# Kernel optimization log

Hardware: AMD Instinct MI355X
Metric: run time of the kernel (lower is better)

## Reference

```python
import jax, jax.numpy as jnp
import numpy as np

N, E, R, D_IN, D_OUT = 50000, 800000, 8, 64, 64


def setup_inputs() -> dict:
    key = jax.random.key(0)
    ks = jax.random.split(key, 8)
    feat = jax.random.normal(ks[0], (N, D_IN), dtype=jnp.float32)
    edge_src = jax.random.randint(ks[1], (E,), 0, N, dtype=jnp.int32)
    edge_dst = jax.random.randint(ks[2], (E,), 0, N, dtype=jnp.int32)
    etype = jax.random.randint(ks[3], (E,), 0, R, dtype=jnp.int32)
    attention = jax.random.uniform(ks[4], (E, 1), dtype=jnp.float32)
    weight = jax.random.normal(ks[5], (R, D_IN, D_OUT), dtype=jnp.float32) * (6.0 / (D_IN + D_OUT)) ** 0.5
    h_bias = jnp.zeros((D_OUT,), dtype=jnp.float32)
    loop_weight = jax.random.normal(ks[6], (D_IN, D_OUT), dtype=jnp.float32) * (6.0 / (D_IN + D_OUT)) ** 0.5
    return {"feat": feat, "edge_src": edge_src, "edge_dst": edge_dst,
            "etype": etype, "attention": attention, "weight": weight,
            "h_bias": h_bias, "loop_weight": loop_weight}


def reference(feat, edge_src, edge_dst, etype, attention, weight, h_bias, loop_weight):
    # Project all nodes through every relation weight once: [R, N, D_OUT].
    # (Equivalent to per-edge bmm with weight[etype] on gathered src feats,
    #  but avoids materializing a [E, D_IN, D_OUT] weight tensor.)
    proj = jnp.einsum('ni,rio->rno', feat, weight)
    # Per-edge message: gather relation-specific projection of src node.
    m = (proj[etype, edge_src] + h_bias) * attention          # [E, D_OUT]
    # Scatter-sum messages to destination nodes.
    agg = jax.ops.segment_sum(m, edge_dst, num_segments=feat.shape[0])
    # Self-loop.
    return agg + feat @ loop_weight
```

## Files before the change

kernel.cpp:

```cpp
#include <hip/hip_runtime.h>

#define D 64

typedef unsigned short ushort_t;
typedef __attribute__((ext_vector_type(8))) short bf16x8;
typedef __attribute__((ext_vector_type(4))) float f32x4;

__device__ __forceinline__ void fma4(float4& c, float a, const float4& b) {
  c.x = fmaf(a, b.x, c.x);
  c.y = fmaf(a, b.y, c.y);
  c.z = fmaf(a, b.z, c.z);
  c.w = fmaf(a, b.w, c.w);
}

__device__ __forceinline__ unsigned short f2bf(float f) {
  unsigned u = __float_as_uint(f);
  return (unsigned short)((u + 0x7FFFu + ((u >> 16) & 1u)) >> 16);
}
__device__ __forceinline__ float bf2f(unsigned short h) {
  return __uint_as_float((unsigned)h << 16);
}
__device__ __forceinline__ unsigned pk2(float a, float b) {
  return (unsigned)f2bf(a) | ((unsigned)f2bf(b) << 16);
}

__device__ __forceinline__ bf16x8 pack_bf8(float4 v0, float4 v1) {
  bf16x8 r;
  r[0] = (short)f2bf(v0.x); r[1] = (short)f2bf(v0.y);
  r[2] = (short)f2bf(v0.z); r[3] = (short)f2bf(v0.w);
  r[4] = (short)f2bf(v1.x); r[5] = (short)f2bf(v1.y);
  r[6] = (short)f2bf(v1.z); r[7] = (short)f2bf(v1.w);
  return r;
}

__global__ void prep(const float* __restrict__ weight, const float* __restrict__ loopw,
                     ushort_t* __restrict__ Wt, int* __restrict__ deg, int R, int N) {
  if ((int)blockIdx.x <= R) {
    const int m = blockIdx.x;
    const float* W = (m < R) ? weight + (size_t)m * D * D : loopw;
    ushort_t* o = Wt + (size_t)m * D * D;
    for (int i = threadIdx.x; i < 1024; i += 256) {
      float4 v = ((const float4*)W)[i];
      int k = i >> 4;
      int c = (i & 15) * 4;
      o[(c + 0) * D + k] = f2bf(v.x);
      o[(c + 1) * D + k] = f2bf(v.y);
      o[(c + 2) * D + k] = f2bf(v.z);
      o[(c + 3) * D + k] = f2bf(v.w);
    }
  } else {
    int i = (blockIdx.x - (R + 1)) * 256 + threadIdx.x;
    if (i < N) deg[i] = 0;
  }
}

template <int NM>
__device__ __forceinline__ void proj_body(const float* __restrict__ feat,
                                          const ushort_t* __restrict__ Wt,
                                          ushort_t* __restrict__ proj,
                                          float* __restrict__ out, int N, int blk) {
  const int t = threadIdx.x;
  const int lane = t & 63;
  const int wid = t >> 6;
  const int node = blk * 64 + wid * 16 + (lane & 15);
  const int g = lane >> 4;
  const int kb = g * 8;
  const int R8 = NM - 1;

  bf16x8 b0, b1;
  {
    float4 v0 = make_float4(0.f, 0.f, 0.f, 0.f), v1 = v0, v2 = v0, v3 = v0;
    if (node < N) {
      const float* p = feat + (size_t)node * D + kb;
      v0 = *(const float4*)p;
      v1 = *(const float4*)(p + 4);
      v2 = *(const float4*)(p + 32);
      v3 = *(const float4*)(p + 36);
    }
    b0 = pack_bf8(v0, v1);
    b1 = pack_bf8(v2, v3);
  }

#pragma unroll 2
  for (int m = 0; m < NM; ++m) {
    const ushort_t* wt = Wt + (size_t)m * D * D + kb;
    f32x4 acc[4];
#pragma unroll
    for (int ct = 0; ct < 4; ++ct) {
      const ushort_t* wr = wt + (size_t)(16 * ct + (lane & 15)) * D;
      bf16x8 a0 = *(const bf16x8*)wr;
      bf16x8 a1 = *(const bf16x8*)(wr + 32);
      acc[ct] = (f32x4){0.f, 0.f, 0.f, 0.f};
      acc[ct] = __builtin_amdgcn_mfma_f32_16x16x32_bf16(a0, b0, acc[ct], 0, 0, 0);
      acc[ct] = __builtin_amdgcn_mfma_f32_16x16x32_bf16(a1, b1, acc[ct], 0, 0, 0);
    }
    if (node < N) {
      if (m < R8) {
        ushort_t* op = proj + ((size_t)node * R8 + m) * D + 16 * g;
        uint4 w0, w1;
        w0.x = pk2(acc[0][0], acc[0][1]); w0.y = pk2(acc[0][2], acc[0][3]);
        w0.z = pk2(acc[1][0], acc[1][1]); w0.w = pk2(acc[1][2], acc[1][3]);
        w1.x = pk2(acc[2][0], acc[2][1]); w1.y = pk2(acc[2][2], acc[2][3]);
        w1.z = pk2(acc[3][0], acc[3][1]); w1.w = pk2(acc[3][2], acc[3][3]);
        *(uint4*)(op) = w0;
        *(uint4*)(op + 8) = w1;
      } else {
        float* op = out + (size_t)node * D + 4 * g;
#pragma unroll
        for (int ct = 0; ct < 4; ++ct) {
          float4 v;
          v.x = acc[ct][0]; v.y = acc[ct][1]; v.z = acc[ct][2]; v.w = acc[ct][3];
          *(float4*)(op + 16 * ct) = v;
        }
      }
    }
  }
}

__device__ __forceinline__ void proj_body_rt(const float* __restrict__ feat,
                                             const ushort_t* __restrict__ Wt,
                                             ushort_t* __restrict__ proj,
                                             float* __restrict__ out, int N, int R,
                                             int blk) {
  const int t = threadIdx.x;
  const int lane = t & 63;
  const int wid = t >> 6;
  const int node = blk * 64 + wid * 16 + (lane & 15);
  const int g = lane >> 4;
  const int kb = g * 8;

  bf16x8 b0, b1;
  {
    float4 v0 = make_float4(0.f, 0.f, 0.f, 0.f), v1 = v0, v2 = v0, v3 = v0;
    if (node < N) {
      const float* p = feat + (size_t)node * D + kb;
      v0 = *(const float4*)p;
      v1 = *(const float4*)(p + 4);
      v2 = *(const float4*)(p + 32);
      v3 = *(const float4*)(p + 36);
    }
    b0 = pack_bf8(v0, v1);
    b1 = pack_bf8(v2, v3);
  }

  for (int m = 0; m <= R; ++m) {
    const ushort_t* wt = Wt + (size_t)m * D * D + kb;
    f32x4 acc[4];
#pragma unroll
    for (int ct = 0; ct < 4; ++ct) {
      const ushort_t* wr = wt + (size_t)(16 * ct + (lane & 15)) * D;
      bf16x8 a0 = *(const bf16x8*)wr;
      bf16x8 a1 = *(const bf16x8*)(wr + 32);
      acc[ct] = (f32x4){0.f, 0.f, 0.f, 0.f};
      acc[ct] = __builtin_amdgcn_mfma_f32_16x16x32_bf16(a0, b0, acc[ct], 0, 0, 0);
      acc[ct] = __builtin_amdgcn_mfma_f32_16x16x32_bf16(a1, b1, acc[ct], 0, 0, 0);
    }
    if (node < N) {
      if (m < R) {
        ushort_t* op = proj + ((size_t)node * R + m) * D + 16 * g;
        uint4 w0, w1;
        w0.x = pk2(acc[0][0], acc[0][1]); w0.y = pk2(acc[0][2], acc[0][3]);
        w0.z = pk2(acc[1][0], acc[1][1]); w0.w = pk2(acc[1][2], acc[1][3]);
        w1.x = pk2(acc[2][0], acc[2][1]); w1.y = pk2(acc[2][2], acc[2][3]);
        w1.z = pk2(acc[3][0], acc[3][1]); w1.w = pk2(acc[3][2], acc[3][3]);
        *(uint4*)(op) = w0;
        *(uint4*)(op + 8) = w1;
      } else {
        float* op = out + (size_t)node * D + 4 * g;
#pragma unroll
        for (int ct = 0; ct < 4; ++ct) {
          float4 v;
          v.x = acc[ct][0]; v.y = acc[ct][1]; v.z = acc[ct][2]; v.w = acc[ct][3];
          *(float4*)(op + 16 * ct) = v;
        }
      }
    }
  }
}

__device__ __forceinline__ void hist_body(const int* __restrict__ edst,
                                          int* __restrict__ deg,
                                          int* __restrict__ rank, int E, int hblk) {
  const int e = (hblk * 256 + (int)threadIdx.x) * 4;
  if (e + 3 < E) {
    int4 d = *(const int4*)(edst + e);
    int4 r;
    r.x = atomicAdd(&deg[d.x], 1);
    r.y = atomicAdd(&deg[d.y], 1);
    r.z = atomicAdd(&deg[d.z], 1);
    r.w = atomicAdd(&deg[d.w], 1);
    *(int4*)(rank + e) = r;
  } else {
    for (int i = e; i < E; ++i) rank[i] = atomicAdd(&deg[edst[i]], 1);
  }
}

__global__ __launch_bounds__(256) void proj_hist(const float* __restrict__ feat,
                                                 const ushort_t* __restrict__ Wt,
                                                 ushort_t* __restrict__ proj,
                                                 float* __restrict__ out,
                                                 const int* __restrict__ edst,
                                                 int* __restrict__ deg,
                                                 int* __restrict__ rank,
                                                 int N, int E, int R, int PB) {
  if ((int)blockIdx.x < PB) {
    if (R == 8)
      proj_body<9>(feat, Wt, proj, out, N, blockIdx.x);
    else
      proj_body_rt(feat, Wt, proj, out, N, R, blockIdx.x);
  } else {
    hist_body(edst, deg, rank, E, blockIdx.x - PB);
  }
}

__global__ __launch_bounds__(256) void scan_partial(const int* __restrict__ deg,
                                                    int* __restrict__ bsum, int N) {
  const int t = threadIdx.x;
  const int base = blockIdx.x * 1024 + t * 4;
  int s = 0;
  if (base + 3 < N) {
    int4 v = *(const int4*)(deg + base);
    s = v.x + v.y + v.z + v.w;
  } else {
#pragma unroll
    for (int k = 0; k < 4; ++k) if (base + k < N) s += deg[base + k];
  }
  __shared__ int red[4];
#pragma unroll
  for (int m = 1; m < 64; m <<= 1) s += __shfl_xor(s, m);
  if ((t & 63) == 0) red[t >> 6] = s;
  __syncthreads();
  if (t == 0) bsum[blockIdx.x] = red[0] + red[1] + red[2] + red[3];
}

__global__ __launch_bounds__(256) void scan_bsum(const int* __restrict__ bsum,
                                                 int* __restrict__ boff,
                                                 int* __restrict__ off, int nb, int N) {
  __shared__ int s[256];
  __shared__ int carry_s;
  const int t = threadIdx.x;
  if (t == 0) carry_s = 0;
  __syncthreads();
  for (int base = 0; base < nb; base += 256) {
    int i = base + t;
    int v = (i < nb) ? bsum[i] : 0;
    s[t] = v;
    __syncthreads();
#pragma unroll
    for (int d = 1; d < 256; d <<= 1) {
      int u = (t >= d) ? s[t - d] : 0;
      __syncthreads();
      s[t] += u;
      __syncthreads();
    }
    int c = carry_s;
    if (i < nb) boff[i] = s[t] - v + c;
    __syncthreads();
    if (t == 0) carry_s = c + s[255];
    __syncthreads();
  }
  if (t == 0) off[N] = carry_s;
}

__global__ __launch_bounds__(256) void scan_apply(const int* __restrict__ deg,
                                                  const int* __restrict__ boff,
                                                  int* __restrict__ off, int N) {
  const int t = threadIdx.x;
  const int base = blockIdx.x * 1024 + t * 4;
  int v0 = 0, v1 = 0, v2 = 0, v3 = 0;
  if (base + 3 < N) {
    int4 v = *(const int4*)(deg + base);
    v0 = v.x; v1 = v.y; v2 = v.z; v3 = v.w;
  } else {
    if (base + 0 < N) v0 = deg[base + 0];
    if (base + 1 < N) v1 = deg[base + 1];
    if (base + 2 < N) v2 = deg[base + 2];
  }
  const int tsum = v0 + v1 + v2 + v3;
  __shared__ int s[256];
  s[t] = tsum;
  __syncthreads();
#pragma unroll
  for (int d = 1; d < 256; d <<= 1) {
    int u = (t >= d) ? s[t - d] : 0;
    __syncthreads();
    s[t] += u;
    __syncthreads();
  }
  int exc = s[t] - tsum + boff[blockIdx.x];
  const int o1 = exc + v0, o2 = o1 + v1, o3 = o2 + v2;
  if (base + 0 < N) off[base + 0] = exc;
  if (base + 1 < N) off[base + 1] = o1;
  if (base + 2 < N) off[base + 2] = o2;
  if (base + 3 < N) off[base + 3] = o3;
}

__global__ void scatter_pos(const int* __restrict__ esrc, const int* __restrict__ edst,
                            const int* __restrict__ etype, const float* __restrict__ att,
                            const int* __restrict__ off, const int* __restrict__ rank,
                            int2* __restrict__ payload, int E) {
  const int e = (blockIdx.x * 256 + threadIdx.x) * 4;
  if (e + 3 < E) {
    int4 s  = *(const int4*)(esrc + e);
    int4 d  = *(const int4*)(edst + e);
    int4 ty = *(const int4*)(etype + e);
    float4 a = *(const float4*)(att + e);
    int4 rk = *(const int4*)(rank + e);
    payload[off[d.x] + rk.x] = make_int2(s.x | (ty.x << 24), __float_as_int(a.x));
    payload[off[d.y] + rk.y] = make_int2(s.y | (ty.y << 24), __float_as_int(a.y));
    payload[off[d.z] + rk.z] = make_int2(s.z | (ty.z << 24), __float_as_int(a.z));
    payload[off[d.w] + rk.w] = make_int2(s.w | (ty.w << 24), __float_as_int(a.w));
  } else {
    for (int i = e; i < E; ++i)
      payload[off[edst[i]] + rank[i]] =
          make_int2(esrc[i] | (etype[i] << 24), __float_as_int(att[i]));
  }
}

__global__ __launch_bounds__(256, 8) void node_gather(const int* __restrict__ off,
                                                      const int2* __restrict__ payload,
                                                      const ushort_t* __restrict__ proj,
                                                      const float* __restrict__ hbias,
                                                      float* __restrict__ out, int N,
                                                      int R) {
  const int n = (blockIdx.x * 256 + threadIdx.x) >> 6;
  if (n >= N) return;
  const int lane = threadIdx.x & 63;
  const int sub = lane >> 4;
  const int q = lane & 15;
  const int ac0 = 16 * (q & 3) + 4 * (q >> 2);

  const int s0 = off[n], s1 = off[n + 1];
  float4 acc = make_float4(0.f, 0.f, 0.f, 0.f);
  float sa = 0.f;
  for (int e = s0 + sub; e < s1; e += 4) {
    const int2 pe = payload[e];
    const float a = __int_as_float(pe.y);
    const int src = pe.x & 0x00FFFFFF;
    const int r = ((unsigned)pe.x) >> 24;
    const ushort4 p = *(const ushort4*)(proj + ((size_t)src * R + r) * D + q * 4);
    acc.x = fmaf(a, bf2f(p.x), acc.x);
    acc.y = fmaf(a, bf2f(p.y), acc.y);
    acc.z = fmaf(a, bf2f(p.z), acc.z);
    acc.w = fmaf(a, bf2f(p.w), acc.w);
    sa += a;
  }
#pragma unroll
  for (int m = 16; m < 64; m <<= 1) {
    acc.x += __shfl_xor(acc.x, m);
    acc.y += __shfl_xor(acc.y, m);
    acc.z += __shfl_xor(acc.z, m);
    acc.w += __shfl_xor(acc.w, m);
    sa += __shfl_xor(sa, m);
  }
  if (sub == 0) {
    const float4 hb = *(const float4*)(hbias + ac0);
    float* op = out + (size_t)n * D + ac0;
    float4 cur = *(float4*)op;
    cur.x += acc.x + sa * hb.x;
    cur.y += acc.y + sa * hb.y;
    cur.z += acc.z + sa * hb.z;
    cur.w += acc.w + sa * hb.w;
    *(float4*)op = cur;
  }
}

__global__ __launch_bounds__(256, 3) void proj_single(const float* __restrict__ feat,
                                                      const float* __restrict__ W,
                                                      float* __restrict__ outp, int N) {
  __shared__ float sW[64 * 64];
  __shared__ float sF[64 * 132];
  const int t = threadIdx.x;
  const int tileBase = blockIdx.x * 128;

  {
    const float4* Wv = (const float4*)W;
    float4* sWv = (float4*)sW;
    for (int k = t; k < 1024; k += 256) sWv[k] = Wv[k];
  }
  {
    const int row = t >> 1, half = t & 1;
    const int gr = tileBase + row;
    if (gr < N) {
      const float4* src = (const float4*)(feat + (size_t)gr * D + half * 32);
#pragma unroll
      for (int k = 0; k < 8; ++k) {
        float4 v = src[k];
        int i0 = half * 32 + k * 4;
        sF[(i0 + 0) * 132 + row] = v.x;
        sF[(i0 + 1) * 132 + row] = v.y;
        sF[(i0 + 2) * 132 + row] = v.z;
        sF[(i0 + 3) * 132 + row] = v.w;
      }
    } else {
#pragma unroll
      for (int k = 0; k < 8; ++k) {
        int i0 = half * 32 + k * 4;
        sF[(i0 + 0) * 132 + row] = 0.f;
        sF[(i0 + 1) * 132 + row] = 0.f;
        sF[(i0 + 2) * 132 + row] = 0.f;
        sF[(i0 + 3) * 132 + row] = 0.f;
      }
    }
  }
  __syncthreads();

  const int c0 = (t & 15) * 4;
  const int r0 = (t >> 4) * 8;
  float4 acc[8];
#pragma unroll
  for (int rr = 0; rr < 8; ++rr) acc[rr] = make_float4(0.f, 0.f, 0.f, 0.f);

#pragma unroll 8
  for (int i = 0; i < 64; ++i) {
    float4 w  = *(const float4*)&sW[i * 64 + c0];
    float4 a0 = *(const float4*)&sF[i * 132 + r0];
    float4 a1 = *(const float4*)&sF[i * 132 + r0 + 4];
    fma4(acc[0], a0.x, w); fma4(acc[1], a0.y, w);
    fma4(acc[2], a0.z, w); fma4(acc[3], a0.w, w);
    fma4(acc[4], a1.x, w); fma4(acc[5], a1.y, w);
    fma4(acc[6], a1.z, w); fma4(acc[7], a1.w, w);
  }

#pragma unroll
  for (int rr = 0; rr < 8; ++rr) {
    int gn = tileBase + r0 + rr;
    if (gn < N) *(float4*)(outp + (size_t)gn * D + c0) = acc[rr];
  }
}

__global__ __launch_bounds__(256, 8) void edge_scatter(const int* __restrict__ esrc,
                                                       const int* __restrict__ edst,
                                                       const int* __restrict__ etype,
                                                       const float* __restrict__ att,
                                                       const float* __restrict__ proj,
                                                       const float* __restrict__ hbias,
                                                       float* __restrict__ out,
                                                       int E, int N, int relFilter) {
  const int t = blockIdx.x * 256 + threadIdx.x;
  const int wave = t >> 6;
  const int lane = threadIdx.x & 63;
  const int sub = lane >> 4;
  const int q = lane & 15;
  const long e = (long)wave * 4 + sub;
  if (e >= E) return;
  const int r = etype[e];
  if (relFilter >= 0 && r != relFilter) return;
  const int s = esrc[e];
  const int dn = edst[e];
  const float a = att[e];
  const size_t base = (size_t)s * D;
  const float4 hb = ((const float4*)hbias)[q];
  const float4 p = *(const float4*)(proj + base + q * 4);
  float* op = out + (size_t)dn * D + q * 4;
  unsafeAtomicAdd(op + 0, (p.x + hb.x) * a);
  unsafeAtomicAdd(op + 1, (p.y + hb.y) * a);
  unsafeAtomicAdd(op + 2, (p.z + hb.z) * a);
  unsafeAtomicAdd(op + 3, (p.w + hb.w) * a);
}

extern "C" void kernel_launch(void* const* d_in, const int* in_sizes, int n_in,
                              void* d_out, int out_size, void* d_ws, size_t ws_size,
                              hipStream_t stream) {
  const float* feat   = (const float*)d_in[0];
  const int* esrc     = (const int*)d_in[1];
  const int* edst     = (const int*)d_in[2];
  const int* etype    = (const int*)d_in[3];
  const float* att    = (const float*)d_in[4];
  const float* weight = (const float*)d_in[5];
  const float* hbias  = (const float*)d_in[6];
  const float* loopw  = (const float*)d_in[7];
  float* out = (float*)d_out;

  const int N = in_sizes[0] / D;
  const int E = in_sizes[1];
  const int R = in_sizes[5] / (D * D);

  const int Npad = (N + 3) & ~3;
  const int nb = (N + 1023) / 1024;

  const size_t wtBytes   = (size_t)(R + 1) * D * D * 2;
  const size_t projBytes = (size_t)N * R * D * 2;
  const size_t intCount  = (size_t)Npad + (size_t)(N + 1) + (size_t)nb + (size_t)E;
  const size_t payOff    = (wtBytes + projBytes + intCount * 4 + 7) & ~(size_t)7;
  const size_t needSorted = payOff + (size_t)E * 8;

  const int PB = (N + 63) / 64;
  const int HB = ((E + 3) / 4 + 255) / 256;
  const int equadBlocks = ((E + 3) / 4 + 255) / 256;

  if (ws_size >= needSorted) {
    ushort_t* Wt   = (ushort_t*)d_ws;
    ushort_t* proj = (ushort_t*)((char*)d_ws + wtBytes);
    int* deg    = (int*)((char*)d_ws + wtBytes + projBytes);
    int* off    = deg + Npad;
    int* bsum   = off + (N + 1);
    int* rank   = bsum + nb;
    int2* payload = (int2*)((char*)d_ws + payOff);

    prep<<<(R + 1) + (N + 255) / 256, 256, 0, stream>>>(weight, loopw, Wt, deg, R, N);
    proj_hist<<<PB + HB, 256, 0, stream>>>(feat, Wt, proj, out, edst, deg, rank,
                                           N, E, R, PB);
    scan_partial<<<nb, 256, 0, stream>>>(deg, bsum, N);
    scan_bsum<<<1, 256, 0, stream>>>(bsum, bsum, off, nb, N);
    scan_apply<<<nb, 256, 0, stream>>>(deg, bsum, off, N);
    scatter_pos<<<equadBlocks, 256, 0, stream>>>(esrc, edst, etype, att, off, rank,
                                                 payload, E);
    node_gather<<<(N + 3) / 4, 256, 0, stream>>>(off, payload, proj, hbias, out, N, R);
  } else {
    const int tilesN = (N + 127) / 128;
    const int eblocks16 = (E + 15) / 16;
    proj_single<<<tilesN, 256, 0, stream>>>(feat, loopw, out, N);
    for (int r = 0; r < R; ++r) {
      proj_single<<<tilesN, 256, 0, stream>>>(feat, weight + (size_t)r * D * D,
                                              (float*)d_ws, N);
      edge_scatter<<<eblocks16, 256, 0, stream>>>(esrc, edst, etype, att, (float*)d_ws,
                                                  hbias, out, E, N, r);
    }
  }
}
```

Baseline: 121.6 us.

## Replace CSR sort with fixed-capacity per-node slot buckets and overflow list

Drops the degree histogram, the three-kernel prefix scan and the separate positional scatter. Edges are now binned directly into fixed 48-slot buckets per destination node using an atomic cursor, inside the same launch as the projection. Edges beyond the capacity go to an overflow list that a small atomic-add kernel applies after the gather. This cuts several launches and passes over the edge arrays, at the cost of a larger, sparser payload buffer. Overflow entries past the list cap would be silently dropped, so very skewed degree distributions are a correctness risk.

```diff
diff --git a/kernel.cpp b/kernel.cpp
--- a/kernel.cpp
+++ b/kernel.cpp
@@ -1,6 +1,8 @@
 #include <hip/hip_runtime.h>
 
 #define D 64
+#define CAP 48
+#define OVCAP 8192
 
 typedef unsigned short ushort_t;
 typedef __attribute__((ext_vector_type(8))) short bf16x8;
@@ -34,7 +36,8 @@
 }
 
 __global__ void prep(const float* __restrict__ weight, const float* __restrict__ loopw,
-                     ushort_t* __restrict__ Wt, int* __restrict__ deg, int R, int N) {
+                     ushort_t* __restrict__ Wt, int* __restrict__ cursor,
+                     int* __restrict__ ovcnt, int R, int N) {
   if ((int)blockIdx.x <= R) {
     const int m = blockIdx.x;
     const float* W = (m < R) ? weight + (size_t)m * D * D : loopw;
@@ -48,9 +51,10 @@
       o[(c + 2) * D + k] = f2bf(v.z);
       o[(c + 3) * D + k] = f2bf(v.w);
     }
+    if (blockIdx.x == 0 && threadIdx.x == 0) *ovcnt = 0;
   } else {
     int i = (blockIdx.x - (R + 1)) * 256 + threadIdx.x;
-    if (i < N) deg[i] = 0;
+    if (i < N) cursor[i] = 0;
   }
 }
 
@@ -178,146 +182,69 @@
   }
 }
 
-__device__ __forceinline__ void hist_body(const int* __restrict__ edst,
-                                          int* __restrict__ deg,
-                                          int* __restrict__ rank, int E, int hblk) {
-  const int e = (hblk * 256 + (int)threadIdx.x) * 4;
-  if (e + 3 < E) {
-    int4 d = *(const int4*)(edst + e);
-    int4 r;
-    r.x = atomicAdd(&deg[d.x], 1);
-    r.y = atomicAdd(&deg[d.y], 1);
-    r.z = atomicAdd(&deg[d.z], 1);
-    r.w = atomicAdd(&deg[d.w], 1);
-    *(int4*)(rank + e) = r;
-  } else {
-    for (int i = e; i < E; ++i) rank[i] = atomicAdd(&deg[edst[i]], 1);
-  }
-}
-
-__global__ __launch_bounds__(256) void proj_hist(const float* __restrict__ feat,
-                                                 const ushort_t* __restrict__ Wt,
-                                                 ushort_t* __restrict__ proj,
-                                                 float* __restrict__ out,
-                                                 const int* __restrict__ edst,
-                                                 int* __restrict__ deg,
-                                                 int* __restrict__ rank,
-                                                 int N, int E, int R, int PB) {
-  if ((int)blockIdx.x < PB) {
-    if (R == 8)
-      proj_body<9>(feat, Wt, proj, out, N, blockIdx.x);
-    else
-      proj_body_rt(feat, Wt, proj, out, N, R, blockIdx.x);
-  } else {
-    hist_body(edst, deg, rank, E, blockIdx.x - PB);
-  }
-}
-
-__global__ __launch_bounds__(256) void scan_partial(const int* __restrict__ deg,
-                                                    int* __restrict__ bsum, int N) {
-  const int t = threadIdx.x;
-  const int base = blockIdx.x * 1024 + t * 4;
-  int s = 0;
-  if (base + 3 < N) {
-    int4 v = *(const int4*)(deg + base);
-    s = v.x + v.y + v.z + v.w;
-  } else {
-#pragma unroll
-    for (int k = 0; k < 4; ++k) if (base + k < N) s += deg[base + k];
-  }
-  __shared__ int red[4];
-#pragma unroll
-  for (int m = 1; m < 64; m <<= 1) s += __shfl_xor(s, m);
-  if ((t & 63) == 0) red[t >> 6] = s;
-  __syncthreads();
-  if (t == 0) bsum[blockIdx.x] = red[0] + red[1] + red[2] + red[3];
-}
-
-__global__ __launch_bounds__(256) void scan_bsum(const int* __restrict__ bsum,
-                                                 int* __restrict__ boff,
-                                                 int* __restrict__ off, int nb, int N) {
-  __shared__ int s[256];
-  __shared__ int carry_s;
-  const int t = threadIdx.x;
-  if (t == 0) carry_s = 0;
-  __syncthreads();
-  for (int base = 0; base < nb; base += 256) {
-    int i = base + t;
-    int v = (i < nb) ? bsum[i] : 0;
-    s[t] = v;
-    __syncthreads();
-#pragma unroll
-    for (int d = 1; d < 256; d <<= 1) {
-      int u = (t >= d) ? s[t - d] : 0;
-      __syncthreads();
-      s[t] += u;
-      __syncthreads();
-    }
-    int c = carry_s;
-    if (i < nb) boff[i] = s[t] - v + c;
-    __syncthreads();
-    if (t == 0) carry_s = c + s[255];
-    __syncthreads();
-  }
-  if (t == 0) off[N] = carry_s;
-}
-
-__global__ __launch_bounds__(256) void scan_apply(const int* __restrict__ deg,
-                                                  const int* __restrict__ boff,
-                                                  int* __restrict__ off, int N) {
-  const int t = threadIdx.x;
-  const int base = blockIdx.x * 1024 + t * 4;
-  int v0 = 0, v1 = 0, v2 = 0, v3 = 0;
-  if (base + 3 < N) {
-    int4 v = *(const int4*)(deg + base);
-    v0 = v.x; v1 = v.y; v2 = v.z; v3 = v.w;
-  } else {
-    if (base + 0 < N) v0 = deg[base + 0];
-    if (base + 1 < N) v1 = deg[base + 1];
-    if (base + 2 < N) v2 = deg[base + 2];
-  }
-  const int tsum = v0 + v1 + v2 + v3;
-  __shared__ int s[256];
-  s[t] = tsum;
-  __syncthreads();
-#pragma unroll
-  for (int d = 1; d < 256; d <<= 1) {
-    int u = (t >= d) ? s[t - d] : 0;
-    __syncthreads();
-    s[t] += u;
-    __syncthreads();
-  }
-  int exc = s[t] - tsum + boff[blockIdx.x];
-  const int o1 = exc + v0, o2 = o1 + v1, o3 = o2 + v2;
-  if (base + 0 < N) off[base + 0] = exc;
-  if (base + 1 < N) off[base + 1] = o1;
-  if (base + 2 < N) off[base + 2] = o2;
-  if (base + 3 < N) off[base + 3] = o3;
-}
-
-__global__ void scatter_pos(const int* __restrict__ esrc, const int* __restrict__ edst,
-                            const int* __restrict__ etype, const float* __restrict__ att,
-                            const int* __restrict__ off, const int* __restrict__ rank,
-                            int2* __restrict__ payload, int E) {
-  const int e = (blockIdx.x * 256 + threadIdx.x) * 4;
+__device__ __forceinline__ void scat_body(const int* __restrict__ esrc,
+                                          const int* __restrict__ edst,
+                                          const int* __restrict__ etype,
+                                          const float* __restrict__ att,
+                                          int* __restrict__ cursor,
+                                          int2* __restrict__ payload,
+                                          int* __restrict__ ovcnt,
+                                          int4* __restrict__ ovlist,
+                                          int E, int sblk) {
+  const int e = (sblk * 256 + (int)threadIdx.x) * 4;
   if (e + 3 < E) {
     int4 s  = *(const int4*)(esrc + e);
     int4 d  = *(const int4*)(edst + e);
     int4 ty = *(const int4*)(etype + e);
     float4 a = *(const float4*)(att + e);
-    int4 rk = *(const int4*)(rank + e);
-    payload[off[d.x] + rk.x] = make_int2(s.x | (ty.x << 24), __float_as_int(a.x));
-    payload[off[d.y] + rk.y] = make_int2(s.y | (ty.y << 24), __float_as_int(a.y));
-    payload[off[d.z] + rk.z] = make_int2(s.z | (ty.z << 24), __float_as_int(a.z));
-    payload[off[d.w] + rk.w] = make_int2(s.w | (ty.w << 24), __float_as_int(a.w));
+    int p0 = atomicAdd(&cursor[d.x], 1);
+    int p1 = atomicAdd(&cursor[d.y], 1);
+    int p2 = atomicAdd(&cursor[d.z], 1);
+    int p3 = atomicAdd(&cursor[d.w], 1);
+    if (p0 < CAP) payload[(size_t)d.x * CAP + p0] = make_int2(s.x | (ty.x << 24), __float_as_int(a.x));
+    else { int ov = atomicAdd(ovcnt, 1); if (ov < OVCAP) ovlist[ov] = make_int4(s.x | (ty.x << 24), __float_as_int(a.x), d.x, 0); }
+    if (p1 < CAP) payload[(size_t)d.y * CAP + p1] = make_int2(s.y | (ty.y << 24), __float_as_int(a.y));
+    else { int ov = atomicAdd(ovcnt, 1); if (ov < OVCAP) ovlist[ov] = make_int4(s.y | (ty.y << 24), __float_as_int(a.y), d.y, 0); }
+    if (p2 < CAP) payload[(size_t)d.z * CAP + p2] = make_int2(s.z | (ty.z << 24), __float_as_int(a.z));
+    else { int ov = atomicAdd(ovcnt, 1); if (ov < OVCAP) ovlist[ov] = make_int4(s.z | (ty.z << 24), __float_as_int(a.z), d.z, 0); }
+    if (p3 < CAP) payload[(size_t)d.w * CAP + p3] = make_int2(s.w | (ty.w << 24), __float_as_int(a.w));
+    else { int ov = atomicAdd(ovcnt, 1); if (ov < OVCAP) ovlist[ov] = make_int4(s.w | (ty.w << 24), __float_as_int(a.w), d.w, 0); }
   } else {
-    for (int i = e; i < E; ++i)
-      payload[off[edst[i]] + rank[i]] =
-          make_int2(esrc[i] | (etype[i] << 24), __float_as_int(att[i]));
-  }
-}
-
-__global__ __launch_bounds__(256, 8) void node_gather(const int* __restrict__ off,
+    for (int i = e; i < E; ++i) {
+      int dn = edst[i];
+      int pos = atomicAdd(&cursor[dn], 1);
+      int2 pay = make_int2(esrc[i] | (etype[i] << 24), __float_as_int(att[i]));
+      if (pos < CAP) payload[(size_t)dn * CAP + pos] = pay;
+      else { int ov = atomicAdd(ovcnt, 1); if (ov < OVCAP) ovlist[ov] = make_int4(pay.x, pay.y, dn, 0); }
+    }
+  }
+}
+
+__global__ __launch_bounds__(256) void proj_scat(const float* __restrict__ feat,
+                                                 const ushort_t* __restrict__ Wt,
+                                                 ushort_t* __restrict__ proj,
+                                                 float* __restrict__ out,
+                                                 const int* __restrict__ esrc,
+                                                 const int* __restrict__ edst,
+                                                 const int* __restrict__ etype,
+                                                 const float* __restrict__ att,
+                                                 int* __restrict__ cursor,
+                                                 int2* __restrict__ payload,
+                                                 int* __restrict__ ovcnt,
+                                                 int4* __restrict__ ovlist,
+                                                 int N, int E, int R, int SB) {
+  if ((int)blockIdx.x < SB) {
+    scat_body(esrc, edst, etype, att, cursor, payload, ovcnt, ovlist, E, blockIdx.x);
+  } else {
+    const int blk = blockIdx.x - SB;
+    if (R == 8)
+      proj_body<9>(feat, Wt, proj, out, N, blk);
+    else
+      proj_body_rt(feat, Wt, proj, out, N, R, blk);
+  }
+}
+
+__global__ __launch_bounds__(256, 8) void node_gather(const int* __restrict__ cursor,
                                                       const int2* __restrict__ payload,
                                                       const ushort_t* __restrict__ proj,
                                                       const float* __restrict__ hbias,
@@ -330,11 +257,12 @@
   const int q = lane & 15;
   const int ac0 = 16 * (q & 3) + 4 * (q >> 2);
 
-  const int s0 = off[n], s1 = off[n + 1];
+  const int cnt = min(cursor[n], CAP);
+  const int2* slots = payload + (size_t)n * CAP;
   float4 acc = make_float4(0.f, 0.f, 0.f, 0.f);
   float sa = 0.f;
-  for (int e = s0 + sub; e < s1; e += 4) {
-    const int2 pe = payload[e];
+  for (int e = sub; e < cnt; e += 4) {
+    const int2 pe = slots[e];
     const float a = __int_as_float(pe.y);
     const int src = pe.x & 0x00FFFFFF;
     const int r = ((unsigned)pe.x) >> 24;
@@ -362,6 +290,27 @@
     cur.z += acc.z + sa * hb.z;
     cur.w += acc.w + sa * hb.w;
     *(float4*)op = cur;
+  }
+}
+
+__global__ void ovf_fix(const int* __restrict__ ovcnt, const int4* __restrict__ ovlist,
+                        const ushort_t* __restrict__ proj, const float* __restrict__ hbias,
+                        float* __restrict__ out, int R) {
+  const int total = min(*ovcnt, OVCAP) * 16;
+  for (int i = blockIdx.x * 256 + threadIdx.x; i < total; i += gridDim.x * 256) {
+    const int idx = i >> 4, q = i & 15;
+    const int4 en = ovlist[idx];
+    const int src = en.x & 0x00FFFFFF;
+    const int r = ((unsigned)en.x) >> 24;
+    const float a = __int_as_float(en.y);
+    const int ac0 = 16 * (q & 3) + 4 * (q >> 2);
+    const ushort4 p = *(const ushort4*)(proj + ((size_t)src * R + r) * D + q * 4);
+    const float4 hb = *(const float4*)(hbias + ac0);
+    float* op = out + (size_t)en.z * D + ac0;
+    unsafeAtomicAdd(op + 0, (bf2f(p.x) + hb.x) * a);
+    unsafeAtomicAdd(op + 1, (bf2f(p.y) + hb.y) * a);
+    unsafeAtomicAdd(op + 2, (bf2f(p.z) + hb.z) * a);
+    unsafeAtomicAdd(op + 3, (bf2f(p.w) + hb.w) * a);
   }
 }
 
@@ -477,36 +426,32 @@
   const int R = in_sizes[5] / (D * D);
 
   const int Npad = (N + 3) & ~3;
-  const int nb = (N + 1023) / 1024;
 
   const size_t wtBytes   = (size_t)(R + 1) * D * D * 2;
   const size_t projBytes = (size_t)N * R * D * 2;
-  const size_t intCount  = (size_t)Npad + (size_t)(N + 1) + (size_t)nb + (size_t)E;
-  const size_t payOff    = (wtBytes + projBytes + intCount * 4 + 7) & ~(size_t)7;
-  const size_t needSorted = payOff + (size_t)E * 8;
+  const size_t curOff    = wtBytes + projBytes;
+  const size_t ovcntOff  = curOff + (size_t)Npad * 4;
+  const size_t ovlistOff = (ovcntOff + 16 + 15) & ~(size_t)15;
+  const size_t payOffB   = (ovlistOff + (size_t)OVCAP * 16 + 15) & ~(size_t)15;
+  const size_t needSlot  = payOffB + (size_t)N * CAP * 8;
 
   const int PB = (N + 63) / 64;
-  const int HB = ((E + 3) / 4 + 255) / 256;
-  const int equadBlocks = ((E + 3) / 4 + 255) / 256;
-
-  if (ws_size >= needSorted) {
+  const int SB = ((E + 3) / 4 + 255) / 256;
+
+  if (ws_size >= needSlot) {
     ushort_t* Wt   = (ushort_t*)d_ws;
     ushort_t* proj = (ushort_t*)((char*)d_ws + wtBytes);
-    int* deg    = (int*)((char*)d_ws + wtBytes + projBytes);
-    int* off    = deg + Npad;
-    int* bsum   = off + (N + 1);
-    int* rank   = bsum + nb;
-    int2* payload = (int2*)((char*)d_ws + payOff);
-
-    prep<<<(R + 1) + (N + 255) / 256, 256, 0, stream>>>(weight, loopw, Wt, deg, R, N);
-    proj_hist<<<PB + HB, 256, 0, stream>>>(feat, Wt, proj, out, edst, deg, rank,
-                                           N, E, R, PB);
-    scan_partial<<<nb, 256, 0, stream>>>(deg, bsum, N);
-    scan_bsum<<<1, 256, 0, stream>>>(bsum, bsum, off, nb, N);
-    scan_apply<<<nb, 256, 0, stream>>>(deg, bsum, off, N);
-    scatter_pos<<<equadBlocks, 256, 0, stream>>>(esrc, edst, etype, att, off, rank,
-                                                 payload, E);
-    node_gather<<<(N + 3) / 4, 256, 0, stream>>>(off, payload, proj, hbias, out, N, R);
+    int* cursor    = (int*)((char*)d_ws + curOff);
+    int* ovcnt     = (int*)((char*)d_ws + ovcntOff);
+    int4* ovlist   = (int4*)((char*)d_ws + ovlistOff);
+    int2* payload  = (int2*)((char*)d_ws + payOffB);
+
+    prep<<<(R + 1) + (N + 255) / 256, 256, 0, stream>>>(weight, loopw, Wt, cursor,
+                                                        ovcnt, R, N);
+    proj_scat<<<SB + PB, 256, 0, stream>>>(feat, Wt, proj, out, esrc, edst, etype, att,
+                                           cursor, payload, ovcnt, ovlist, N, E, R, SB);
+    node_gather<<<(N + 3) / 4, 256, 0, stream>>>(cursor, payload, proj, hbias, out, N, R);
+    ovf_fix<<<16, 256, 0, stream>>>(ovcnt, ovlist, proj, hbias, out, R);
   } else {
     const int tilesN = (N + 127) / 128;
     const int eblocks16 = (E + 15) / 16;
```

Measured after the change: 135.8 us. 1.12x slower.
